# Performance work log

Hardware: AMD Instinct MI355X
Metric: run time of the kernel (lower is better)

Reference implementation:

```python
import jax, jax.numpy as jnp
import numpy as np

B, L, D, H, DK, DV = 2, 2048, 512, 8, 64, 64
EPS = 1e-6


def setup_inputs() -> dict:
    key = jax.random.key(0)
    ks = jax.random.split(key, 19)
    n = lambda k, s: jax.random.normal(k, s, dtype=jnp.float32)
    inp = {
        "q_r": n(ks[0], (B, L, D)), "q_i": n(ks[1], (B, L, D)),
        "k_r": n(ks[2], (B, L, D)), "k_i": n(ks[3], (B, L, D)),
        "v_r": n(ks[4], (B, L, D)), "v_i": n(ks[5], (B, L, D)),
        "wq_r": n(ks[6], (D, H * DK)) * 0.02, "wq_i": n(ks[7], (D, H * DK)) * 0.02,
        "wk_r": n(ks[8], (D, H * DK)) * 0.02, "wk_i": n(ks[9], (D, H * DK)) * 0.02,
        "wv_r": n(ks[10], (D, H * DV)) * 0.02, "wv_i": n(ks[11], (D, H * DV)) * 0.02,
        "wo_r": n(ks[12], (H * DV, D)) * 0.02, "wo_i": n(ks[13], (H * DV, D)) * 0.02,
        "ln_wr": n(ks[14], (D,)), "ln_wi": n(ks[15], (D,)),
        "ln_br": n(ks[16], (D,)), "ln_bi": n(ks[17], (D,)),
        "mask": jax.random.randint(ks[18], (B, L, L), 0, 2).astype(jnp.int32),
    }
    return inp


def _clinear(xr, xi, wr, wi):
    # complex matmul (xr + i xi) @ (wr + i wi)
    return xr @ wr - xi @ wi, xi @ wr + xr @ wi


def _complex_layernorm(r, i, wr, wi, br, bi, eps=EPS):
    axes = (1, 2)  # normalize over all non-batch dims of [B, L, D]
    r = r - r.mean(axis=axes, keepdims=True)
    i = i - i.mean(axis=axes, keepdims=True)
    Crr = (r * r).mean(axis=axes, keepdims=True) + eps
    Cii = (i * i).mean(axis=axes, keepdims=True) + eps
    Cri = (r * i).mean(axis=axes, keepdims=True)
    s = jnp.sqrt(Crr * Cii - Cri * Cri)
    t = jnp.sqrt(Crr + Cii + 2.0 * s)
    inv_st = 1.0 / (s * t)
    Rrr = (Cii + s) * inv_st
    Rii = (Crr + s) * inv_st
    Rri = -Cri * inv_st
    nr = Rrr * r + Rri * i
    ni = Rii * i + Rri * r
    # affine: complex multiply by (wr + i wi), then add complex bias
    out_r = nr * wr - ni * wi + br
    out_i = nr * wi + ni * wr + bi
    return out_r, out_i


def reference(q_r, q_i, k_r, k_i, v_r, v_i,
              wq_r, wq_i, wk_r, wk_i, wv_r, wv_i, wo_r, wo_i,
              ln_wr, ln_wi, ln_br, ln_bi, mask):
    res_r, res_i = q_r, q_i
    qr, qi = _clinear(q_r, q_i, wq_r, wq_i)
    kr, ki = _clinear(k_r, k_i, wk_r, wk_i)
    vr, vi = _clinear(v_r, v_i, wv_r, wv_i)
    # [B, L, H*Dk] -> [B, H, L, Dk]
    tohead = lambda x, d: x.reshape(B, L, H, d).transpose(0, 2, 1, 3)
    qr, qi = tohead(qr, DK), tohead(qi, DK)
    kr, ki = tohead(kr, DK), tohead(ki, DK)
    vr, vi = tohead(vr, DV), tohead(vi, DV)
    temp = jnp.float32(DK) ** 0.5
    qr, qi = qr / temp, qi / temp
    # complex scores (q @ conj(k)^T): re + i*im
    sr = jnp.einsum('bhqd,bhkd->bhqk', qr, kr) + jnp.einsum('bhqd,bhkd->bhqk', qi, ki)
    si = jnp.einsum('bhqd,bhkd->bhqk', qi, kr) - jnp.einsum('bhqd,bhkd->bhqk', qr, ki)
    a = jnp.sqrt(sr * sr + si * si)  # abs of complex scores
    a = jnp.where(mask[:, None, :, :] == 0, jnp.float32(-1e9), a)
    attn = jax.nn.softmax(a, axis=-1)  # real-valued attention weights
    out_r = jnp.einsum('bhqk,bhkd->bhqd', attn, vr)
    out_i = jnp.einsum('bhqk,bhkd->bhqd', attn, vi)
    # [B, H, L, Dv] -> [B, L, H*Dv]
    out_r = out_r.transpose(0, 2, 1, 3).reshape(B, L, H * DV)
    out_i = out_i.transpose(0, 2, 1, 3).reshape(B, L, H * DV)
    out_r, out_i = _clinear(out_r, out_i, wo_r, wo_i)
    out_r = out_r + res_r
    out_i = out_i + res_i
    out_r, out_i = _complex_layernorm(out_r, out_i, ln_wr, ln_wi, ln_br, ln_bi)
    return out_r, out_i, attn
```

## Files before the change

### kernel.cpp

```cpp
#include <hip/hip_runtime.h>

typedef unsigned short u16;
typedef unsigned int u32;
typedef unsigned long long u64;


typedef __attribute__((ext_vector_type(8))) short bf16x8;
typedef __attribute__((ext_vector_type(4))) float f32x4;
typedef __attribute__((ext_vector_type(4))) u32 u32x4;

__device__ __forceinline__ u16 f2bf(float f) {
  u32 x = __float_as_uint(f);
  return (u16)((x + 0x7FFFu + ((x >> 16) & 1u)) >> 16);
}
__device__ __forceinline__ u32 pk2(float a, float b) {
  return (u32)f2bf(a) | ((u32)f2bf(b) << 16);
}
__device__ __forceinline__ bf16x8 negv(bf16x8 v) {
  u32x4 x = __builtin_bit_cast(u32x4, v);
  x ^= 0x80008000u;
  return __builtin_bit_cast(bf16x8, x);
}

__global__ __launch_bounds__(256) void prep(
    const float* __restrict__ qr, const float* __restrict__ qi,
    const float* __restrict__ kr, const float* __restrict__ ki,
    const float* __restrict__ vr, const float* __restrict__ vi,
    const float* __restrict__ wqr, const float* __restrict__ wqi,
    const float* __restrict__ wkr, const float* __restrict__ wki,
    const float* __restrict__ wvr, const float* __restrict__ wvi,
    const float* __restrict__ wor, const float* __restrict__ woi,
    const int* __restrict__ mask,
    u16* __restrict__ A, u16* __restrict__ Btb, u64* __restrict__ mb,
    float* __restrict__ stats) {
  __shared__ float tile[64][65];
  int bid = blockIdx.x;
  int t = threadIdx.x;
  if (bid < 32768) {
    int tid = bid * 256 + t;
    u64 bal = __ballot(mask[tid] != 0);
    if ((t & 63) == 0) mb[tid >> 6] = bal;
    return;
  }
  bid -= 32768;
  if (bid < 6144) {
    int z = bid >> 11;
    int bx = bid & 2047;
    const float* r  = (z == 0) ? qr : (z == 1) ? kr : vr;
    const float* im = (z == 0) ? qi : (z == 1) ? ki : vi;
    int c = bx * 256 + t;
    int m = c >> 7;
    int ck = (c & 127) * 8;
    const float* s = (ck < 512) ? (r + (size_t)m * 512 + ck)
                                : (im + (size_t)m * 512 + (ck - 512));
    float4 a = ((const float4*)s)[0];
    float4 b = ((const float4*)s)[1];
    uint4 o;
    o.x = pk2(a.x, a.y); o.y = pk2(a.z, a.w);
    o.z = pk2(b.x, b.y); o.w = pk2(b.z, b.w);
    ((uint4*)(A + (size_t)z * 4194304))[c] = o;
    return;
  }
  bid -= 6144;
  if (bid < 1024) {
    int z = bid >> 8;
    int bx = bid & 255;
    const float* wr = (z==0)?wqr:(z==1)?wkr:(z==2)?wvr:wor;
    const float* wi = (z==0)?wqi:(z==1)?wki:(z==2)?wvi:woi;
    u16* Bt = Btb + (size_t)z * 1048576;
    int n0 = (bx >> 4) * 64;
    int k0 = (bx & 15) * 64;
    bool nlow = (n0 < 512), klow = (k0 < 512);
    const float* src = nlow ? (klow ? wr : wi) : (klow ? wi : wr);
    float sgn = (nlow && !klow) ? -1.0f : 1.0f;
    int col0 = nlow ? n0 : n0 - 512;
    int kr0 = klow ? k0 : k0 - 512;
    {
      int rr = t >> 2, cc = (t & 3) * 16;
      const float4* s = (const float4*)(src + (size_t)(kr0 + rr) * 512 + col0 + cc);
#pragma unroll
      for (int j = 0; j < 4; ++j) {
        float4 v = s[j];
        tile[rr][cc + j*4 + 0] = v.x; tile[rr][cc + j*4 + 1] = v.y;
        tile[rr][cc + j*4 + 2] = v.z; tile[rr][cc + j*4 + 3] = v.w;
      }
    }
    __syncthreads();
    {
      int nn = t >> 2, kc = (t & 3) * 16;
      u32 w[8];
#pragma unroll
      for (int j = 0; j < 8; ++j)
        w[j] = pk2(sgn * tile[kc + 2*j][nn], sgn * tile[kc + 2*j + 1][nn]);
      uint4* d = (uint4*)(Bt + (size_t)(n0 + nn) * 1024 + k0 + kc);
      d[0] = make_uint4(w[0], w[1], w[2], w[3]);
      d[1] = make_uint4(w[4], w[5], w[6], w[7]);
    }
    return;
  }
  if (t < 16) stats[t] = 0.0f;
}

__global__ __launch_bounds__(256) void pack_vt(const u16* __restrict__ Cvm,
                                               u16* __restrict__ vt) {
  int z = blockIdx.y;
  int b = z >> 3, h = z & 7;
  int lt = blockIdx.x >> 1, ct = blockIdx.x & 1;
  int l0 = lt * 64, c0 = ct * 64;
  int n0 = (ct == 0) ? (h * 64) : (512 + h * 64);
  __shared__ u16 tile[64][80];
  int t = threadIdx.x;
  {
    int lr = t >> 2, cc = (t & 3) * 16;
    const uint4* s = (const uint4*)(Cvm + ((size_t)(b * 2048 + l0 + lr)) * 1024 + n0 + cc);
    uint4 v0 = s[0], v1 = s[1];
    *(uint4*)&tile[lr][cc] = v0;
    *(uint4*)&tile[lr][cc + 8] = v1;
  }
  __syncthreads();
  {
    int cr = t >> 2, lc = (t & 3) * 16;
    u32 w[8];
#pragma unroll
    for (int j = 0; j < 8; ++j)
      w[j] = (u32)tile[lc + 2*j][cr] | ((u32)tile[lc + 2*j + 1][cr] << 16);
    uint4* d = (uint4*)(vt + ((size_t)z * 128 + c0 + cr) * 2048 + l0 + lc);
    d[0] = make_uint4(w[0], w[1], w[2], w[3]);
    d[1] = make_uint4(w[4], w[5], w[6], w[7]);
  }
}

__device__ __forceinline__ void glds128(const u16* __restrict__ g, int ld,
                                        u16* lds, int t) {
  int lane = t & 63, w = t >> 6;
  int sub = lane >> 3;
  int cs = (lane & 7) ^ sub;
#pragma unroll
  for (int p = 0; p < 4; ++p) {
    int r = p * 32 + w * 8 + sub;
    const u16* ga = g + (size_t)r * ld + cs * 8;
    u16* la = lds + (size_t)(p * 32 + w * 8) * 64;
    __builtin_amdgcn_global_load_lds(
        (const __attribute__((address_space(1))) void*)ga,
        (__attribute__((address_space(3))) void*)la, 16, 0, 0);
  }
}
__device__ __forceinline__ void glds64(const u16* __restrict__ g, int ld,
                                       u16* lds, int t) {
  int lane = t & 63, w = t >> 6;
  int sub = lane >> 3;
  int cs = (lane & 7) ^ sub;
#pragma unroll
  for (int p = 0; p < 2; ++p) {
    int r = p * 32 + w * 8 + sub;
    const u16* ga = g + (size_t)r * ld + cs * 8;
    u16* la = lds + (size_t)(p * 32 + w * 8) * 64;
    __builtin_amdgcn_global_load_lds(
        (const __attribute__((address_space(1))) void*)ga,
        (__attribute__((address_space(3))) void*)la, 16, 0, 0);
  }
}

__global__ __launch_bounds__(256) void gemm_proj(const u16* __restrict__ Abase,
                                                 const u16* __restrict__ Btbase,
                                                 u16* __restrict__ Cbase) {
  __shared__ u16 lA[128 * 64], lB[128 * 64];
  int t = threadIdx.x, lane = t & 63, wid = t >> 6;
  int c15 = lane & 15, g = lane >> 4, l7 = lane & 7;
  int z = blockIdx.z;
  const u16* A  = Abase  + (size_t)z * 4194304;
  const u16* Bt = Btbase + (size_t)z * 1048576;
  u16* C = Cbase + (size_t)z * 4194304;
  int brow = blockIdx.y * 128, bcol = blockIdx.x * 128;
  float scale = (z == 0) ? 0.125f : 1.0f;
  int sw0 = ((g ^ l7) << 3), sw1 = (((4 | g) ^ l7) << 3);
  int wr0 = (wid >> 1) * 64 + c15, wc0 = (wid & 1) * 64 + c15;
  const u16 *pA0 = lA + wr0 * 64 + sw0, *pA1 = lA + wr0 * 64 + sw1;
  const u16 *pB0 = lB + wc0 * 64 + sw0, *pB1 = lB + wc0 * 64 + sw1;
  f32x4 zero = {0.f, 0.f, 0.f, 0.f};
  f32x4 acc[4][4];
#pragma unroll
  for (int mi = 0; mi < 4; ++mi)
#pragma unroll
    for (int ni = 0; ni < 4; ++ni) acc[mi][ni] = zero;
  for (int kt = 0; kt < 1024; kt += 64) {
    glds128(A + (size_t)brow * 1024 + kt, 1024, lA, t);
    glds128(Bt + (size_t)bcol * 1024 + kt, 1024, lB, t);
    __syncthreads();
#pragma unroll
    for (int ks = 0; ks < 2; ++ks) {
      const u16* pa = ks ? pA1 : pA0;
      const u16* pb = ks ? pB1 : pB0;
      bf16x8 fa[4], fb[4];
#pragma unroll
      for (int i2 = 0; i2 < 4; ++i2) {
        fa[i2] = *(const bf16x8*)(pa + i2 * 1024);
        fb[i2] = *(const bf16x8*)(pb + i2 * 1024);
      }
#pragma unroll
      for (int mi = 0; mi < 4; ++mi)
#pragma unroll
        for (int ni = 0; ni < 4; ++ni)
          acc[mi][ni] = __builtin_amdgcn_mfma_f32_16x16x32_bf16(
              fa[mi], fb[ni], acc[mi][ni], 0, 0, 0);
    }
    __syncthreads();
  }
  int wrb = (wid >> 1) * 64, wcb = (wid & 1) * 64;
  int rj = g * 4, cj = c15;
#pragma unroll
  for (int mi = 0; mi < 4; ++mi)
#pragma unroll
    for (int ni = 0; ni < 4; ++ni)
#pragma unroll
      for (int j = 0; j < 4; ++j)
        C[(size_t)(brow + wrb + mi * 16 + rj + j) * 1024 +
          (bcol + wcb + ni * 16 + cj)] = f2bf(acc[mi][ni][j] * scale);
}

__global__ __launch_bounds__(256, 3) void fused_p1(
    const u16* __restrict__ Cq, const u16* __restrict__ Ck,
    const u16* __restrict__ vt, const u64* __restrict__ mb,
    float* __restrict__ invbuf, u16* __restrict__ Ao) {
  __shared__ u16 lKr[64 * 64], lKi[64 * 64], lV[128 * 64], lP[64 * 64];
  int t = threadIdx.x, lane = t & 63, w = t >> 6;
  int c15 = lane & 15, g = lane >> 4, l7 = lane & 7;
  int f = blockIdx.x + (int)gridDim.x * blockIdx.y;
  int wk = (f & 7) * 64 + (f >> 3);
  int strip = wk & 31, z = wk >> 5;
  int b = z >> 3, h = z & 7;
  int q0 = strip * 64;
  int arow = w * 16 + c15;
  int rbase = w * 16 + (g << 2);

  const u16* Qrow = Cq + ((size_t)(b * 2048 + q0 + arow)) * 1024 + h * 64;
  bf16x8 q0r = *(const bf16x8*)(Qrow + g * 8);
  bf16x8 q1r = *(const bf16x8*)(Qrow + 32 + g * 8);
  bf16x8 q0i = *(const bf16x8*)(Qrow + 512 + g * 8);
  bf16x8 q1i = *(const bf16x8*)(Qrow + 544 + g * 8);
  bf16x8 nq0r = negv(q0r), nq1r = negv(q1r);

  int sw0 = ((g ^ l7) << 3), sw1 = (((4 | g) ^ l7) << 3);
  const u16 *pKr0 = lKr + c15 * 64 + sw0, *pKr1 = lKr + c15 * 64 + sw1;
  const u16 *pKi0 = lKi + c15 * 64 + sw0, *pKi1 = lKi + c15 * 64 + sw1;
  const u16 *pV0 = lV + c15 * 64 + sw0, *pV1 = lV + c15 * 64 + sw1;
  const u16 *pP0 = lP + arow * 64 + sw0, *pP1 = lP + arow * 64 + sw1;

  size_t mbase = ((size_t)(b * 2048 + q0 + rbase)) * 32;
  float s[4] = {0.f, 0.f, 0.f, 0.f};
  f32x4 zero = {0.f, 0.f, 0.f, 0.f};
  f32x4 o[8];
#pragma unroll
  for (int ni = 0; ni < 8; ++ni) o[ni] = zero;

  const u16* Kb = Ck + ((size_t)(b * 2048)) * 1024 + h * 64;
  const u16* Vb = vt + (size_t)z * 262144;

  for (int tl = 0; tl < 32; ++tl) {
    int l0 = tl * 64;
    if (tl) __syncthreads();
    glds64(Kb + (size_t)l0 * 1024, 1024, lKr, t);
    glds64(Kb + (size_t)l0 * 1024 + 512, 1024, lKi, t);
    glds128(Vb + l0, 2048, lV, t);
    __syncthreads();
    f32x4 sr[4], si[4];
#pragma unroll
    for (int ni = 0; ni < 4; ++ni) { sr[ni] = zero; si[ni] = zero; }
#pragma unroll
    for (int ni = 0; ni < 4; ++ni) {
      bf16x8 g0 = *(const bf16x8*)(pKr0 + ni * 1024);
      bf16x8 g1 = *(const bf16x8*)(pKi0 + ni * 1024);
      sr[ni] = __builtin_amdgcn_mfma_f32_16x16x32_bf16(q0r, g0, sr[ni], 0, 0, 0);
      sr[ni] = __builtin_amdgcn_mfma_f32_16x16x32_bf16(q0i, g1, sr[ni], 0, 0, 0);
      si[ni] = __builtin_amdgcn_mfma_f32_16x16x32_bf16(q0i, g0, si[ni], 0, 0, 0);
      si[ni] = __builtin_amdgcn_mfma_f32_16x16x32_bf16(nq0r, g1, si[ni], 0, 0, 0);
      bf16x8 h0 = *(const bf16x8*)(pKr1 + ni * 1024);
      bf16x8 h1 = *(const bf16x8*)(pKi1 + ni * 1024);
      sr[ni] = __builtin_amdgcn_mfma_f32_16x16x32_bf16(q1r, h0, sr[ni], 0, 0, 0);
      sr[ni] = __builtin_amdgcn_mfma_f32_16x16x32_bf16(q1i, h1, sr[ni], 0, 0, 0);
      si[ni] = __builtin_amdgcn_mfma_f32_16x16x32_bf16(q1i, h0, si[ni], 0, 0, 0);
      si[ni] = __builtin_amdgcn_mfma_f32_16x16x32_bf16(nq1r, h1, si[ni], 0, 0, 0);
    }
    u64 wm[4];
#pragma unroll
    for (int j = 0; j < 4; ++j) wm[j] = mb[mbase + (size_t)j * 32 + tl];
#pragma unroll
    for (int ni = 0; ni < 4; ++ni) {
      int cbit = ni * 16 + c15;
      int pchi = ni * 2 + (c15 >> 3);
#pragma unroll
      for (int j = 0; j < 4; ++j) {
        float n = sr[ni][j] * sr[ni][j] + si[ni][j] * si[ni][j];
        float p = __expf(__builtin_amdgcn_sqrtf(n));
        p = ((wm[j] >> cbit) & 1ull) ? p : 0.0f;
        s[j] += p;
        lP[(rbase + j) * 64 + ((pchi ^ (((g & 1) << 2) + j)) << 3) + l7] = f2bf(p);
      }
    }
    {
      bf16x8 fa0 = *(const bf16x8*)pP0;
      bf16x8 fa1 = *(const bf16x8*)pP1;
#pragma unroll
      for (int ni = 0; ni < 8; ++ni) {
        bf16x8 fb0 = *(const bf16x8*)(pV0 + ni * 1024);
        bf16x8 fb1 = *(const bf16x8*)(pV1 + ni * 1024);
        o[ni] = __builtin_amdgcn_mfma_f32_16x16x32_bf16(fa0, fb0, o[ni], 0, 0, 0);
        o[ni] = __builtin_amdgcn_mfma_f32_16x16x32_bf16(fa1, fb1, o[ni], 0, 0, 0);
      }
    }
  }
  float inv[4];
#pragma unroll
  for (int j = 0; j < 4; ++j) {
    float sj = s[j];
#pragma unroll
    for (int off = 1; off < 16; off <<= 1) sj += __shfl_xor(sj, off);
    inv[j] = 1.0f / sj;
  }
  if (c15 == 0) {
#pragma unroll
    for (int j = 0; j < 4; ++j)
      invbuf[z * 2048 + q0 + rbase + j] = inv[j];
  }
#pragma unroll
  for (int ni = 0; ni < 8; ++ni) {
    int c = ni * 16 + c15;
    int nout = (c < 64) ? (h * 64 + c) : (512 + h * 64 + (c - 64));
#pragma unroll
    for (int j = 0; j < 4; ++j)
      Ao[((size_t)(b * 2048 + q0 + rbase + j)) * 1024 + nout] =
          f2bf(o[ni][j] * inv[j]);
  }
}

__global__ __launch_bounds__(256, 3) void attn_p2(
    const u16* __restrict__ Cq, const u16* __restrict__ Ck,
    const u64* __restrict__ mb, const float* __restrict__ invbuf,
    float* __restrict__ attn) {
  __shared__ u16 lKr[64 * 64], lKi[64 * 64];
  int t = threadIdx.x, lane = t & 63, w = t >> 6;
  int c15 = lane & 15, g = lane >> 4, l7 = lane & 7;
  int f = blockIdx.x + (int)gridDim.x * blockIdx.y;
  int wk = (f & 7) * 256 + (f >> 3);
  int z = wk >> 7;
  int rem = wk & 127;
  int strip = rem >> 2, kc = rem & 3;
  int b = z >> 3, h = z & 7;
  int q0 = strip * 64;
  int arow = w * 16 + c15;
  int rbase = w * 16 + (g << 2);

  const u16* Qrow = Cq + ((size_t)(b * 2048 + q0 + arow)) * 1024 + h * 64;
  bf16x8 q0r = *(const bf16x8*)(Qrow + g * 8);
  bf16x8 q1r = *(const bf16x8*)(Qrow + 32 + g * 8);
  bf16x8 q0i = *(const bf16x8*)(Qrow + 512 + g * 8);
  bf16x8 q1i = *(const bf16x8*)(Qrow + 544 + g * 8);
  bf16x8 nq0r = negv(q0r), nq1r = negv(q1r);

  int sw0 = ((g ^ l7) << 3), sw1 = (((4 | g) ^ l7) << 3);
  const u16 *pKr0 = lKr + c15 * 64 + sw0, *pKr1 = lKr + c15 * 64 + sw1;
  const u16 *pKi0 = lKi + c15 * 64 + sw0, *pKi1 = lKi + c15 * 64 + sw1;

  size_t mbase = ((size_t)(b * 2048 + q0 + rbase)) * 32;
  float inv[4];
#pragma unroll
  for (int j = 0; j < 4; ++j) inv[j] = invbuf[z * 2048 + q0 + rbase + j];
  f32x4 zero = {0.f, 0.f, 0.f, 0.f};
  const u16* Kb = Ck + ((size_t)(b * 2048)) * 1024 + h * 64;
  float* arow_out = attn + ((size_t)z * 2048 + q0 + rbase) * 2048 + c15;

  for (int tt2 = 0; tt2 < 8; ++tt2) {
    int tl = kc * 8 + tt2;
    int l0 = tl * 64;
    if (tt2) __syncthreads();
    glds64(Kb + (size_t)l0 * 1024, 1024, lKr, t);
    glds64(Kb + (size_t)l0 * 1024 + 512, 1024, lKi, t);
    __syncthreads();
    f32x4 sr[4], si[4];
#pragma unroll
    for (int ni = 0; ni < 4; ++ni) { sr[ni] = zero; si[ni] = zero; }
#pragma unroll
    for (int ni = 0; ni < 4; ++ni) {
      bf16x8 g0 = *(const bf16x8*)(pKr0 + ni * 1024);
      bf16x8 g1 = *(const bf16x8*)(pKi0 + ni * 1024);
      sr[ni] = __builtin_amdgcn_mfma_f32_16x16x32_bf16(q0r, g0, sr[ni], 0, 0, 0);
      sr[ni] = __builtin_amdgcn_mfma_f32_16x16x32_bf16(q0i, g1, sr[ni], 0, 0, 0);
      si[ni] = __builtin_amdgcn_mfma_f32_16x16x32_bf16(q0i, g0, si[ni], 0, 0, 0);
      si[ni] = __builtin_amdgcn_mfma_f32_16x16x32_bf16(nq0r, g1, si[ni], 0, 0, 0);
      bf16x8 h0 = *(const bf16x8*)(pKr1 + ni * 1024);
      bf16x8 h1 = *(const bf16x8*)(pKi1 + ni * 1024);
      sr[ni] = __builtin_amdgcn_mfma_f32_16x16x32_bf16(q1r, h0, sr[ni], 0, 0, 0);
      sr[ni] = __builtin_amdgcn_mfma_f32_16x16x32_bf16(q1i, h1, sr[ni], 0, 0, 0);
      si[ni] = __builtin_amdgcn_mfma_f32_16x16x32_bf16(q1i, h0, si[ni], 0, 0, 0);
      si[ni] = __builtin_amdgcn_mfma_f32_16x16x32_bf16(nq1r, h1, si[ni], 0, 0, 0);
    }
    u64 wm[4];
#pragma unroll
    for (int j = 0; j < 4; ++j) wm[j] = mb[mbase + (size_t)j * 32 + tl];
    float* outp = arow_out + l0;
#pragma unroll
    for (int ni = 0; ni < 4; ++ni) {
      int cbit = ni * 16 + c15;
#pragma unroll
      for (int j = 0; j < 4; ++j) {
        float n = sr[ni][j] * sr[ni][j] + si[ni][j] * si[ni][j];
        float p = __expf(__builtin_amdgcn_sqrtf(n)) * inv[j];
        p = ((wm[j] >> cbit) & 1ull) ? p : 0.0f;
        outp[(size_t)j * 2048 + ni * 16] = p;
      }
    }
  }
}

__global__ __launch_bounds__(256) void gemm_oproj(
    const u16* __restrict__ A, const u16* __restrict__ Bt,
    const float* __restrict__ resR, const float* __restrict__ resI,
    float* __restrict__ outR, float* __restrict__ outI) {
  __shared__ u16 lA[128 * 64], lB[128 * 64];
  int t = threadIdx.x, lane = t & 63, wid = t >> 6;
  int c15 = lane & 15, g = lane >> 4, l7 = lane & 7;
  int brow = blockIdx.y * 128, bcol = blockIdx.x * 128;
  int sw0 = ((g ^ l7) << 3), sw1 = (((4 | g) ^ l7) << 3);
  int wr0 = (wid >> 1) * 64 + c15, wc0 = (wid & 1) * 64 + c15;
  const u16 *pA0 = lA + wr0 * 64 + sw0, *pA1 = lA + wr0 * 64 + sw1;
  const u16 *pB0 = lB + wc0 * 64 + sw0, *pB1 = lB + wc0 * 64 + sw1;
  f32x4 zero = {0.f, 0.f, 0.f, 0.f};
  f32x4 acc[4][4];
#pragma unroll
  for (int mi = 0; mi < 4; ++mi)
#pragma unroll
    for (int ni = 0; ni < 4; ++ni) acc[mi][ni] = zero;
  for (int kt = 0; kt < 1024; kt += 64) {
    glds128(A + (size_t)brow * 1024 + kt, 1024, lA, t);
    glds128(Bt + (size_t)bcol * 1024 + kt, 1024, lB, t);
    __syncthreads();
#pragma unroll
    for (int ks = 0; ks < 2; ++ks) {
      const u16* pa = ks ? pA1 : pA0;
      const u16* pb = ks ? pB1 : pB0;
      bf16x8 fa[4], fb[4];
#pragma unroll
      for (int i2 = 0; i2 < 4; ++i2) {
        fa[i2] = *(const bf16x8*)(pa + i2 * 1024);
        fb[i2] = *(const bf16x8*)(pb + i2 * 1024);
      }
#pragma unroll
      for (int mi = 0; mi < 4; ++mi)
#pragma unroll
        for (int ni = 0; ni < 4; ++ni)
          acc[mi][ni] = __builtin_amdgcn_mfma_f32_16x16x32_bf16(
              fa[mi], fb[ni], acc[mi][ni], 0, 0, 0);
    }
    __syncthreads();
  }
  int wrb = (wid >> 1) * 64, wcb = (wid & 1) * 64;
  int rj = g * 4, cj = c15;
#pragma unroll
  for (int mi = 0; mi < 4; ++mi)
#pragma unroll
    for (int ni = 0; ni < 4; ++ni)
#pragma unroll
      for (int j = 0; j < 4; ++j) {
        int row = brow + wrb + mi * 16 + rj + j;
        int col = bcol + wcb + ni * 16 + cj;
        float v = acc[mi][ni][j];
        if (col < 512)
          outR[(size_t)row * 512 + col] = v + resR[(size_t)row * 512 + col];
        else {
          int c2 = col - 512;
          outI[(size_t)row * 512 + c2] = v + resI[(size_t)row * 512 + c2];
        }
      }
}

__global__ __launch_bounds__(256) void ln_reduce(const float* __restrict__ outR,
                                                 const float* __restrict__ outI,
                                                 float* __restrict__ stats) {
  int b = blockIdx.y;
  int t = threadIdx.x;
  size_t base = (size_t)b * 1048576 + (size_t)blockIdx.x * 2048;
  float s0 = 0.f, s1 = 0.f, s2 = 0.f, s3 = 0.f, s4 = 0.f;
#pragma unroll
  for (int p = 0; p < 8; ++p) {
    size_t e = base + p * 256 + t;
    float r = outR[e], i = outI[e];
    s0 += r; s1 += i; s2 += r * r; s3 += i * i; s4 += r * i;
  }
#pragma unroll
  for (int off = 32; off; off >>= 1) {
    s0 += __shfl_xor(s0, off); s1 += __shfl_xor(s1, off);
    s2 += __shfl_xor(s2, off); s3 += __shfl_xor(s3, off);
    s4 += __shfl_xor(s4, off);
  }
  __shared__ float red[4][5];
  if ((t & 63) == 0) {
    int w = t >> 6;
    red[w][0] = s0; red[w][1] = s1; red[w][2] = s2; red[w][3] = s3; red[w][4] = s4;
  }
  __syncthreads();
  if (t == 0) {
    float a0 = red[0][0] + red[1][0] + red[2][0] + red[3][0];
    float a1 = red[0][1] + red[1][1] + red[2][1] + red[3][1];
    float a2 = red[0][2] + red[1][2] + red[2][2] + red[3][2];
    float a3 = red[0][3] + red[1][3] + red[2][3] + red[3][3];
    float a4 = red[0][4] + red[1][4] + red[2][4] + red[3][4];
    atomicAdd(&stats[b * 8 + 0], a0);
    atomicAdd(&stats[b * 8 + 1], a1);
    atomicAdd(&stats[b * 8 + 2], a2);
    atomicAdd(&stats[b * 8 + 3], a3);
    atomicAdd(&stats[b * 8 + 4], a4);
  }
}

__global__ __launch_bounds__(256) void ln_apply(
    float* __restrict__ outR, float* __restrict__ outI,
    const float* __restrict__ stats,
    const float* __restrict__ lnwr, const float* __restrict__ lnwi,
    const float* __restrict__ lnbr, const float* __restrict__ lnbi) {
  int b = blockIdx.y;
  const float* st = stats + b * 8;
  float iN = 1.0f / 1048576.0f;
  float mr = st[0] * iN, mi = st[1] * iN;
  float Crr = st[2] * iN - mr * mr + 1e-6f;
  float Cii = st[3] * iN - mi * mi + 1e-6f;
  float Cri = st[4] * iN - mr * mi;
  float s = sqrtf(fmaxf(Crr * Cii - Cri * Cri, 0.f));
  float tt = sqrtf(Crr + Cii + 2.f * s);
  float inv = 1.0f / (s * tt);
  float Rrr = (Cii + s) * inv, Rii = (Crr + s) * inv, Rri = -Cri * inv;
  size_t e = ((size_t)blockIdx.x * 256 + threadIdx.x) * 4;
  size_t idx = (size_t)b * 1048576 + e;
  int d = (int)(e & 511);
  float4 r4 = *(float4*)(outR + idx);
  float4 i4 = *(float4*)(outI + idx);
  float4 wr = *(const float4*)(lnwr + d);
  float4 wi = *(const float4*)(lnwi + d);
  float4 br = *(const float4*)(lnbr + d);
  float4 bi = *(const float4*)(lnbi + d);
  float4 orr, oii;
#pragma unroll
  for (int j = 0; j < 4; ++j) {
    float r = ((&r4.x)[j]) - mr;
    float i = ((&i4.x)[j]) - mi;
    float nr = Rrr * r + Rri * i;
    float ni = Rii * i + Rri * r;
    (&orr.x)[j] = nr * (&wr.x)[j] - ni * (&wi.x)[j] + (&br.x)[j];
    (&oii.x)[j] = nr * (&wi.x)[j] + ni * (&wr.x)[j] + (&bi.x)[j];
  }
  *(float4*)(outR + idx) = orr;
  *(float4*)(outI + idx) = oii;
}

extern "C" void kernel_launch(void* const* d_in, const int* in_sizes, int n_in,
                              void* d_out, int out_size, void* d_ws, size_t ws_size,
                              hipStream_t stream) {
  const float* q_r = (const float*)d_in[0];
  const float* q_i = (const float*)d_in[1];
  const float* k_r = (const float*)d_in[2];
  const float* k_i = (const float*)d_in[3];
  const float* v_r = (const float*)d_in[4];
  const float* v_i = (const float*)d_in[5];
  const float* wq_r = (const float*)d_in[6];
  const float* wq_i = (const float*)d_in[7];
  const float* wk_r = (const float*)d_in[8];
  const float* wk_i = (const float*)d_in[9];
  const float* wv_r = (const float*)d_in[10];
  const float* wv_i = (const float*)d_in[11];
  const float* wo_r = (const float*)d_in[12];
  const float* wo_i = (const float*)d_in[13];
  const float* ln_wr = (const float*)d_in[14];
  const float* ln_wi = (const float*)d_in[15];
  const float* ln_br = (const float*)d_in[16];
  const float* ln_bi = (const float*)d_in[17];
  const int* mask = (const int*)d_in[18];

  float* outR = (float*)d_out;
  float* outI = outR + 2097152;
  float* attn = outR + 4194304;

  char* ws = (char*)d_ws;
  u16* Aq = (u16*)ws;
  u16* Bt = (u16*)(ws + 25165824);
  u16* Cq = (u16*)(ws + 33554432);
  u16* Ck = Cq + 4194304;
  u16* Cv = Cq + 8388608;
  u16* vt = Aq;
  u16* Ao = (u16*)(ws + 58720256);
  u64* mb = (u64*)(ws + 67108864);
  float* stats = (float*)(ws + 69206016);
  float* invbuf = (float*)(ws + 69207040);

  prep<<<dim3(32768 + 6144 + 1024 + 1), 256, 0, stream>>>(
      q_r, q_i, k_r, k_i, v_r, v_i, wq_r, wq_i, wk_r, wk_i, wv_r, wv_i,
      wo_r, wo_i, mask, Aq, Bt, mb, stats);
  gemm_proj<<<dim3(8, 32, 3), 256, 0, stream>>>(Aq, Bt, Cq);
  pack_vt<<<dim3(64, 16), 256, 0, stream>>>(Cv, vt);
  fused_p1<<<dim3(32, 16), 256, 0, stream>>>(Cq, Ck, vt, mb, invbuf, Ao);
  attn_p2<<<dim3(128, 16), 256, 0, stream>>>(Cq, Ck, mb, invbuf, attn);
  gemm_oproj<<<dim3(8, 32), 256, 0, stream>>>(Ao, Bt + 3145728, q_r, q_i, outR, outI);
  ln_reduce<<<dim3(512, 2), 256, 0, stream>>>(outR, outI, stats);
  ln_apply<<<dim3(1024, 2), 256, 0, stream>>>(outR, outI, stats, ln_wr, ln_wi,
                                              ln_br, ln_bi);
}
```

Before: 338.1 us.

## Double-buffer K/V shared-memory tiles in attention kernels to prefetch next tile

Both attention passes now keep two LDS buffers for the K (and V) tiles. Each iteration issues the load for tile t+1 before computing on tile t, which replaces the two barriers per iteration with one. The aim is to hide global-to-LDS load latency behind the MFMA and softmax work. In exchange, LDS use roughly doubles, and fused_p1's launch bound drops from 3 to 2 blocks per CU, which lowers occupancy.

After: 339.4 us. No clear change (+0.4%).

```diff
diff --git a/kernel.cpp b/kernel.cpp
--- a/kernel.cpp
+++ b/kernel.cpp
@@ -218,11 +218,11 @@
           (bcol + wcb + ni * 16 + cj)] = f2bf(acc[mi][ni][j] * scale);
 }
 
-__global__ __launch_bounds__(256, 3) void fused_p1(
+__global__ __launch_bounds__(256, 2) void fused_p1(
     const u16* __restrict__ Cq, const u16* __restrict__ Ck,
     const u16* __restrict__ vt, const u64* __restrict__ mb,
     float* __restrict__ invbuf, u16* __restrict__ Ao) {
-  __shared__ u16 lKr[64 * 64], lKi[64 * 64], lV[128 * 64], lP[64 * 64];
+  __shared__ u16 lKr[2][4096], lKi[2][4096], lV[2][8192], lP[4096];
   int t = threadIdx.x, lane = t & 63, w = t >> 6;
   int c15 = lane & 15, g = lane >> 4, l7 = lane & 7;
   int f = blockIdx.x + (int)gridDim.x * blockIdx.y;
@@ -241,9 +241,12 @@
   bf16x8 nq0r = negv(q0r), nq1r = negv(q1r);
 
   int sw0 = ((g ^ l7) << 3), sw1 = (((4 | g) ^ l7) << 3);
-  const u16 *pKr0 = lKr + c15 * 64 + sw0, *pKr1 = lKr + c15 * 64 + sw1;
-  const u16 *pKi0 = lKi + c15 * 64 + sw0, *pKi1 = lKi + c15 * 64 + sw1;
-  const u16 *pV0 = lV + c15 * 64 + sw0, *pV1 = lV + c15 * 64 + sw1;
+  const u16 *pKr0a = lKr[0] + c15 * 64 + sw0, *pKr1a = lKr[0] + c15 * 64 + sw1;
+  const u16 *pKr0b = lKr[1] + c15 * 64 + sw0, *pKr1b = lKr[1] + c15 * 64 + sw1;
+  const u16 *pKi0a = lKi[0] + c15 * 64 + sw0, *pKi1a = lKi[0] + c15 * 64 + sw1;
+  const u16 *pKi0b = lKi[1] + c15 * 64 + sw0, *pKi1b = lKi[1] + c15 * 64 + sw1;
+  const u16 *pV0a = lV[0] + c15 * 64 + sw0, *pV1a = lV[0] + c15 * 64 + sw1;
+  const u16 *pV0b = lV[1] + c15 * 64 + sw0, *pV1b = lV[1] + c15 * 64 + sw1;
   const u16 *pP0 = lP + arow * 64 + sw0, *pP1 = lP + arow * 64 + sw1;
 
   size_t mbase = ((size_t)(b * 2048 + q0 + rbase)) * 32;
@@ -256,26 +259,35 @@
   const u16* Kb = Ck + ((size_t)(b * 2048)) * 1024 + h * 64;
   const u16* Vb = vt + (size_t)z * 262144;
 
+  glds64(Kb, 1024, lKr[0], t);
+  glds64(Kb + 512, 1024, lKi[0], t);
+  glds128(Vb, 2048, lV[0], t);
+  __syncthreads();
+
   for (int tl = 0; tl < 32; ++tl) {
-    int l0 = tl * 64;
-    if (tl) __syncthreads();
-    glds64(Kb + (size_t)l0 * 1024, 1024, lKr, t);
-    glds64(Kb + (size_t)l0 * 1024 + 512, 1024, lKi, t);
-    glds128(Vb + l0, 2048, lV, t);
-    __syncthreads();
+    int cur = tl & 1;
+    if (tl < 31) {
+      size_t l1 = (size_t)(tl + 1) * 64;
+      glds64(Kb + l1 * 1024, 1024, lKr[cur ^ 1], t);
+      glds64(Kb + l1 * 1024 + 512, 1024, lKi[cur ^ 1], t);
+      glds128(Vb + l1, 2048, lV[cur ^ 1], t);
+    }
+    const u16 *kr0 = cur ? pKr0b : pKr0a, *kr1 = cur ? pKr1b : pKr1a;
+    const u16 *ki0 = cur ? pKi0b : pKi0a, *ki1 = cur ? pKi1b : pKi1a;
+    const u16 *v0p = cur ? pV0b : pV0a, *v1p = cur ? pV1b : pV1a;
     f32x4 sr[4], si[4];
 #pragma unroll
     for (int ni = 0; ni < 4; ++ni) { sr[ni] = zero; si[ni] = zero; }
 #pragma unroll
     for (int ni = 0; ni < 4; ++ni) {
-      bf16x8 g0 = *(const bf16x8*)(pKr0 + ni * 1024);
-      bf16x8 g1 = *(const bf16x8*)(pKi0 + ni * 1024);
+      bf16x8 g0 = *(const bf16x8*)(kr0 + ni * 1024);
+      bf16x8 g1 = *(const bf16x8*)(ki0 + ni * 1024);
       sr[ni] = __builtin_amdgcn_mfma_f32_16x16x32_bf16(q0r, g0, sr[ni], 0, 0, 0);
       sr[ni] = __builtin_amdgcn_mfma_f32_16x16x32_bf16(q0i, g1, sr[ni], 0, 0, 0);
       si[ni] = __builtin_amdgcn_mfma_f32_16x16x32_bf16(q0i, g0, si[ni], 0, 0, 0);
       si[ni] = __builtin_amdgcn_mfma_f32_16x16x32_bf16(nq0r, g1, si[ni], 0, 0, 0);
-      bf16x8 h0 = *(const bf16x8*)(pKr1 + ni * 1024);
-      bf16x8 h1 = *(const bf16x8*)(pKi1 + ni * 1024);
+      bf16x8 h0 = *(const bf16x8*)(kr1 + ni * 1024);
+      bf16x8 h1 = *(const bf16x8*)(ki1 + ni * 1024);
       sr[ni] = __builtin_amdgcn_mfma_f32_16x16x32_bf16(q1r, h0, sr[ni], 0, 0, 0);
       sr[ni] = __builtin_amdgcn_mfma_f32_16x16x32_bf16(q1i, h1, sr[ni], 0, 0, 0);
       si[ni] = __builtin_amdgcn_mfma_f32_16x16x32_bf16(q1i, h0, si[ni], 0, 0, 0);
@@ -302,12 +314,13 @@
       bf16x8 fa1 = *(const bf16x8*)pP1;
 #pragma unroll
       for (int ni = 0; ni < 8; ++ni) {
-        bf16x8 fb0 = *(const bf16x8*)(pV0 + ni * 1024);
-        bf16x8 fb1 = *(const bf16x8*)(pV1 + ni * 1024);
+        bf16x8 fb0 = *(const bf16x8*)(v0p + ni * 1024);
+        bf16x8 fb1 = *(const bf16x8*)(v1p + ni * 1024);
         o[ni] = __builtin_amdgcn_mfma_f32_16x16x32_bf16(fa0, fb0, o[ni], 0, 0, 0);
         o[ni] = __builtin_amdgcn_mfma_f32_16x16x32_bf16(fa1, fb1, o[ni], 0, 0, 0);
       }
     }
+    if (tl < 31) __syncthreads();
   }
   float inv[4];
 #pragma unroll
@@ -337,7 +350,7 @@
     const u16* __restrict__ Cq, const u16* __restrict__ Ck,
     const u64* __restrict__ mb, const float* __restrict__ invbuf,
     float* __restrict__ attn) {
-  __shared__ u16 lKr[64 * 64], lKi[64 * 64];
+  __shared__ u16 lKr[2][4096], lKi[2][4096];
   int t = threadIdx.x, lane = t & 63, w = t >> 6;
   int c15 = lane & 15, g = lane >> 4, l7 = lane & 7;
   int f = blockIdx.x + (int)gridDim.x * blockIdx.y;
@@ -358,8 +371,10 @@
   bf16x8 nq0r = negv(q0r), nq1r = negv(q1r);
 
   int sw0 = ((g ^ l7) << 3), sw1 = (((4 | g) ^ l7) << 3);
-  const u16 *pKr0 = lKr + c15 * 64 + sw0, *pKr1 = lKr + c15 * 64 + sw1;
-  const u16 *pKi0 = lKi + c15 * 64 + sw0, *pKi1 = lKi + c15 * 64 + sw1;
+  const u16 *pKr0a = lKr[0] + c15 * 64 + sw0, *pKr1a = lKr[0] + c15 * 64 + sw1;
+  const u16 *pKr0b = lKr[1] + c15 * 64 + sw0, *pKr1b = lKr[1] + c15 * 64 + sw1;
+  const u16 *pKi0a = lKi[0] + c15 * 64 + sw0, *pKi1a = lKi[0] + c15 * 64 + sw1;
+  const u16 *pKi0b = lKi[1] + c15 * 64 + sw0, *pKi1b = lKi[1] + c15 * 64 + sw1;
 
   size_t mbase = ((size_t)(b * 2048 + q0 + rbase)) * 32;
   float inv[4];
@@ -369,26 +384,37 @@
   const u16* Kb = Ck + ((size_t)(b * 2048)) * 1024 + h * 64;
   float* arow_out = attn + ((size_t)z * 2048 + q0 + rbase) * 2048 + c15;
 
+  {
+    size_t l0 = (size_t)(kc * 8) * 64;
+    glds64(Kb + l0 * 1024, 1024, lKr[0], t);
+    glds64(Kb + l0 * 1024 + 512, 1024, lKi[0], t);
+  }
+  __syncthreads();
+
   for (int tt2 = 0; tt2 < 8; ++tt2) {
     int tl = kc * 8 + tt2;
     int l0 = tl * 64;
-    if (tt2) __syncthreads();
-    glds64(Kb + (size_t)l0 * 1024, 1024, lKr, t);
-    glds64(Kb + (size_t)l0 * 1024 + 512, 1024, lKi, t);
-    __syncthreads();
+    int cur = tt2 & 1;
+    if (tt2 < 7) {
+      size_t l1 = (size_t)(tl + 1) * 64;
+      glds64(Kb + l1 * 1024, 1024, lKr[cur ^ 1], t);
+      glds64(Kb + l1 * 1024 + 512, 1024, lKi[cur ^ 1], t);
+    }
+    const u16 *kr0 = cur ? pKr0b : pKr0a, *kr1 = cur ? pKr1b : pKr1a;
+    const u16 *ki0 = cur ? pKi0b : pKi0a, *ki1 = cur ? pKi1b : pKi1a;
     f32x4 sr[4], si[4];
 #pragma unroll
     for (int ni = 0; ni < 4; ++ni) { sr[ni] = zero; si[ni] = zero; }
 #pragma unroll
     for (int ni = 0; ni < 4; ++ni) {
-      bf16x8 g0 = *(const bf16x8*)(pKr0 + ni * 1024);
-      bf16x8 g1 = *(const bf16x8*)(pKi0 + ni * 1024);
+      bf16x8 g0 = *(const bf16x8*)(kr0 + ni * 1024);
+      bf16x8 g1 = *(const bf16x8*)(ki0 + ni * 1024);
       sr[ni] = __builtin_amdgcn_mfma_f32_16x16x32_bf16(q0r, g0, sr[ni], 0, 0, 0);
       sr[ni] = __builtin_amdgcn_mfma_f32_16x16x32_bf16(q0i, g1, sr[ni], 0, 0, 0);
       si[ni] = __builtin_amdgcn_mfma_f32_16x16x32_bf16(q0i, g0, si[ni], 0, 0, 0);
       si[ni] = __builtin_amdgcn_mfma_f32_16x16x32_bf16(nq0r, g1, si[ni], 0, 0, 0);
-      bf16x8 h0 = *(const bf16x8*)(pKr1 + ni * 1024);
-      bf16x8 h1 = *(const bf16x8*)(pKi1 + ni * 1024);
+      bf16x8 h0 = *(const bf16x8*)(kr1 + ni * 1024);
+      bf16x8 h1 = *(const bf16x8*)(ki1 + ni * 1024);
       sr[ni] = __builtin_amdgcn_mfma_f32_16x16x32_bf16(q1r, h0, sr[ni], 0, 0, 0);
       sr[ni] = __builtin_amdgcn_mfma_f32_16x16x32_bf16(q1i, h1, sr[ni], 0, 0, 0);
       si[ni] = __builtin_amdgcn_mfma_f32_16x16x32_bf16(q1i, h0, si[ni], 0, 0, 0);
@@ -409,6 +435,7 @@
         outp[(size_t)j * 2048 + ni * 16] = p;
       }
     }
+    if (tt2 < 7) __syncthreads();
   }
 }
 
```

## Fuse V transpose into projection GEMM and co-schedule attn pass2 with output GEMM

Applied to the files above, without the earlier changes.

The V projection GEMM now writes its bf16 result straight into the transposed per-head vt layout, so the separate pack_vt kernel and its round trip through memory go away. The attention-probability pass and the output projection GEMM, which are independent of each other, are merged into one launch with a block-index split. The output GEMM blocks can then fill the GPU alongside the memory-bound attn writes, and one launch is saved. vt moves to a new workspace offset. The cost is scattered 8-byte transposed stores in the GEMM epilogue, and the merged kernel drops the occupancy hint of 3 blocks.

After: 355.8 us. 5.3% more time.

```diff
diff --git a/kernel.cpp b/kernel.cpp
--- a/kernel.cpp
+++ b/kernel.cpp
@@ -101,35 +101,6 @@
   if (t < 16) stats[t] = 0.0f;
 }
 
-__global__ __launch_bounds__(256) void pack_vt(const u16* __restrict__ Cvm,
-                                               u16* __restrict__ vt) {
-  int z = blockIdx.y;
-  int b = z >> 3, h = z & 7;
-  int lt = blockIdx.x >> 1, ct = blockIdx.x & 1;
-  int l0 = lt * 64, c0 = ct * 64;
-  int n0 = (ct == 0) ? (h * 64) : (512 + h * 64);
-  __shared__ u16 tile[64][80];
-  int t = threadIdx.x;
-  {
-    int lr = t >> 2, cc = (t & 3) * 16;
-    const uint4* s = (const uint4*)(Cvm + ((size_t)(b * 2048 + l0 + lr)) * 1024 + n0 + cc);
-    uint4 v0 = s[0], v1 = s[1];
-    *(uint4*)&tile[lr][cc] = v0;
-    *(uint4*)&tile[lr][cc + 8] = v1;
-  }
-  __syncthreads();
-  {
-    int cr = t >> 2, lc = (t & 3) * 16;
-    u32 w[8];
-#pragma unroll
-    for (int j = 0; j < 8; ++j)
-      w[j] = (u32)tile[lc + 2*j][cr] | ((u32)tile[lc + 2*j + 1][cr] << 16);
-    uint4* d = (uint4*)(vt + ((size_t)z * 128 + c0 + cr) * 2048 + l0 + lc);
-    d[0] = make_uint4(w[0], w[1], w[2], w[3]);
-    d[1] = make_uint4(w[4], w[5], w[6], w[7]);
-  }
-}
-
 __device__ __forceinline__ void glds128(const u16* __restrict__ g, int ld,
                                         u16* lds, int t) {
   int lane = t & 63, w = t >> 6;
@@ -163,7 +134,8 @@
 
 __global__ __launch_bounds__(256) void gemm_proj(const u16* __restrict__ Abase,
                                                  const u16* __restrict__ Btbase,
-                                                 u16* __restrict__ Cbase) {
+                                                 u16* __restrict__ Cbase,
+                                                 u16* __restrict__ vt) {
   __shared__ u16 lA[128 * 64], lB[128 * 64];
   int t = threadIdx.x, lane = t & 63, wid = t >> 6;
   int c15 = lane & 15, g = lane >> 4, l7 = lane & 7;
@@ -208,14 +180,32 @@
   }
   int wrb = (wid >> 1) * 64, wcb = (wid & 1) * 64;
   int rj = g * 4, cj = c15;
-#pragma unroll
-  for (int mi = 0; mi < 4; ++mi)
-#pragma unroll
-    for (int ni = 0; ni < 4; ++ni)
-#pragma unroll
-      for (int j = 0; j < 4; ++j)
-        C[(size_t)(brow + wrb + mi * 16 + rj + j) * 1024 +
-          (bcol + wcb + ni * 16 + cj)] = f2bf(acc[mi][ni][j] * scale);
+  if (z != 2) {
+#pragma unroll
+    for (int mi = 0; mi < 4; ++mi)
+#pragma unroll
+      for (int ni = 0; ni < 4; ++ni)
+#pragma unroll
+        for (int j = 0; j < 4; ++j)
+          C[(size_t)(brow + wrb + mi * 16 + rj + j) * 1024 +
+            (bcol + wcb + ni * 16 + cj)] = f2bf(acc[mi][ni][j] * scale);
+  } else {
+    int bq = brow >> 11;
+    int lq = (brow & 2047) + wrb + rj;
+#pragma unroll
+    for (int mi = 0; mi < 4; ++mi)
+#pragma unroll
+      for (int ni = 0; ni < 4; ++ni) {
+        int col = bcol + wcb + ni * 16 + cj;
+        int h = (col < 512) ? (col >> 6) : ((col - 512) >> 6);
+        int c = (col & 63) + ((col < 512) ? 0 : 64);
+        ushort4 v4;
+        v4.x = f2bf(acc[mi][ni][0]); v4.y = f2bf(acc[mi][ni][1]);
+        v4.z = f2bf(acc[mi][ni][2]); v4.w = f2bf(acc[mi][ni][3]);
+        *(ushort4*)(vt + ((size_t)((bq * 8 + h) * 128 + c)) * 2048 +
+                    lq + mi * 16) = v4;
+      }
+  }
 }
 
 __global__ __launch_bounds__(256, 3) void fused_p1(
@@ -333,144 +323,147 @@
   }
 }
 
-__global__ __launch_bounds__(256, 3) void attn_p2(
+__global__ __launch_bounds__(256) void tail_k(
     const u16* __restrict__ Cq, const u16* __restrict__ Ck,
     const u64* __restrict__ mb, const float* __restrict__ invbuf,
-    float* __restrict__ attn) {
-  __shared__ u16 lKr[64 * 64], lKi[64 * 64];
-  int t = threadIdx.x, lane = t & 63, w = t >> 6;
+    float* __restrict__ attn, const u16* __restrict__ Ao,
+    const u16* __restrict__ BtO, const float* __restrict__ resR,
+    const float* __restrict__ resI, float* __restrict__ outR,
+    float* __restrict__ outI) {
+  __shared__ u16 shm[16384];
+  int t = threadIdx.x, lane = t & 63;
   int c15 = lane & 15, g = lane >> 4, l7 = lane & 7;
-  int f = blockIdx.x + (int)gridDim.x * blockIdx.y;
-  int wk = (f & 7) * 256 + (f >> 3);
-  int z = wk >> 7;
-  int rem = wk & 127;
-  int strip = rem >> 2, kc = rem & 3;
-  int b = z >> 3, h = z & 7;
-  int q0 = strip * 64;
-  int arow = w * 16 + c15;
-  int rbase = w * 16 + (g << 2);
-
-  const u16* Qrow = Cq + ((size_t)(b * 2048 + q0 + arow)) * 1024 + h * 64;
-  bf16x8 q0r = *(const bf16x8*)(Qrow + g * 8);
-  bf16x8 q1r = *(const bf16x8*)(Qrow + 32 + g * 8);
-  bf16x8 q0i = *(const bf16x8*)(Qrow + 512 + g * 8);
-  bf16x8 q1i = *(const bf16x8*)(Qrow + 544 + g * 8);
-  bf16x8 nq0r = negv(q0r), nq1r = negv(q1r);
-
   int sw0 = ((g ^ l7) << 3), sw1 = (((4 | g) ^ l7) << 3);
-  const u16 *pKr0 = lKr + c15 * 64 + sw0, *pKr1 = lKr + c15 * 64 + sw1;
-  const u16 *pKi0 = lKi + c15 * 64 + sw0, *pKi1 = lKi + c15 * 64 + sw1;
-
-  size_t mbase = ((size_t)(b * 2048 + q0 + rbase)) * 32;
-  float inv[4];
-#pragma unroll
-  for (int j = 0; j < 4; ++j) inv[j] = invbuf[z * 2048 + q0 + rbase + j];
+  int f = blockIdx.x;
   f32x4 zero = {0.f, 0.f, 0.f, 0.f};
-  const u16* Kb = Ck + ((size_t)(b * 2048)) * 1024 + h * 64;
-  float* arow_out = attn + ((size_t)z * 2048 + q0 + rbase) * 2048 + c15;
-
-  for (int tt2 = 0; tt2 < 8; ++tt2) {
-    int tl = kc * 8 + tt2;
-    int l0 = tl * 64;
-    if (tt2) __syncthreads();
-    glds64(Kb + (size_t)l0 * 1024, 1024, lKr, t);
-    glds64(Kb + (size_t)l0 * 1024 + 512, 1024, lKi, t);
-    __syncthreads();
-    f32x4 sr[4], si[4];
-#pragma unroll
-    for (int ni = 0; ni < 4; ++ni) { sr[ni] = zero; si[ni] = zero; }
-#pragma unroll
-    for (int ni = 0; ni < 4; ++ni) {
-      bf16x8 g0 = *(const bf16x8*)(pKr0 + ni * 1024);
-      bf16x8 g1 = *(const bf16x8*)(pKi0 + ni * 1024);
-      sr[ni] = __builtin_amdgcn_mfma_f32_16x16x32_bf16(q0r, g0, sr[ni], 0, 0, 0);
-      sr[ni] = __builtin_amdgcn_mfma_f32_16x16x32_bf16(q0i, g1, sr[ni], 0, 0, 0);
-      si[ni] = __builtin_amdgcn_mfma_f32_16x16x32_bf16(q0i, g0, si[ni], 0, 0, 0);
-      si[ni] = __builtin_amdgcn_mfma_f32_16x16x32_bf16(nq0r, g1, si[ni], 0, 0, 0);
-      bf16x8 h0 = *(const bf16x8*)(pKr1 + ni * 1024);
-      bf16x8 h1 = *(const bf16x8*)(pKi1 + ni * 1024);
-      sr[ni] = __builtin_amdgcn_mfma_f32_16x16x32_bf16(q1r, h0, sr[ni], 0, 0, 0);
-      sr[ni] = __builtin_amdgcn_mfma_f32_16x16x32_bf16(q1i, h1, sr[ni], 0, 0, 0);
-      si[ni] = __builtin_amdgcn_mfma_f32_16x16x32_bf16(q1i, h0, si[ni], 0, 0, 0);
-      si[ni] = __builtin_amdgcn_mfma_f32_16x16x32_bf16(nq1r, h1, si[ni], 0, 0, 0);
-    }
-    u64 wm[4];
-#pragma unroll
-    for (int j = 0; j < 4; ++j) wm[j] = mb[mbase + (size_t)j * 32 + tl];
-    float* outp = arow_out + l0;
-#pragma unroll
-    for (int ni = 0; ni < 4; ++ni) {
-      int cbit = ni * 16 + c15;
-#pragma unroll
-      for (int j = 0; j < 4; ++j) {
-        float n = sr[ni][j] * sr[ni][j] + si[ni][j] * si[ni][j];
-        float p = __expf(__builtin_amdgcn_sqrtf(n)) * inv[j];
-        p = ((wm[j] >> cbit) & 1ull) ? p : 0.0f;
-        outp[(size_t)j * 2048 + ni * 16] = p;
-      }
-    }
-  }
-}
-
-__global__ __launch_bounds__(256) void gemm_oproj(
-    const u16* __restrict__ A, const u16* __restrict__ Bt,
-    const float* __restrict__ resR, const float* __restrict__ resI,
-    float* __restrict__ outR, float* __restrict__ outI) {
-  __shared__ u16 lA[128 * 64], lB[128 * 64];
-  int t = threadIdx.x, lane = t & 63, wid = t >> 6;
-  int c15 = lane & 15, g = lane >> 4, l7 = lane & 7;
-  int brow = blockIdx.y * 128, bcol = blockIdx.x * 128;
-  int sw0 = ((g ^ l7) << 3), sw1 = (((4 | g) ^ l7) << 3);
-  int wr0 = (wid >> 1) * 64 + c15, wc0 = (wid & 1) * 64 + c15;
-  const u16 *pA0 = lA + wr0 * 64 + sw0, *pA1 = lA + wr0 * 64 + sw1;
-  const u16 *pB0 = lB + wc0 * 64 + sw0, *pB1 = lB + wc0 * 64 + sw1;
-  f32x4 zero = {0.f, 0.f, 0.f, 0.f};
-  f32x4 acc[4][4];
-#pragma unroll
-  for (int mi = 0; mi < 4; ++mi)
-#pragma unroll
-    for (int ni = 0; ni < 4; ++ni) acc[mi][ni] = zero;
-  for (int kt = 0; kt < 1024; kt += 64) {
-    glds128(A + (size_t)brow * 1024 + kt, 1024, lA, t);
-    glds128(Bt + (size_t)bcol * 1024 + kt, 1024, lB, t);
-    __syncthreads();
-#pragma unroll
-    for (int ks = 0; ks < 2; ++ks) {
-      const u16* pa = ks ? pA1 : pA0;
-      const u16* pb = ks ? pB1 : pB0;
-      bf16x8 fa[4], fb[4];
-#pragma unroll
-      for (int i2 = 0; i2 < 4; ++i2) {
-        fa[i2] = *(const bf16x8*)(pa + i2 * 1024);
-        fb[i2] = *(const bf16x8*)(pb + i2 * 1024);
-      }
-#pragma unroll
-      for (int mi = 0; mi < 4; ++mi)
-#pragma unroll
-        for (int ni = 0; ni < 4; ++ni)
-          acc[mi][ni] = __builtin_amdgcn_mfma_f32_16x16x32_bf16(
-              fa[mi], fb[ni], acc[mi][ni], 0, 0, 0);
-    }
-    __syncthreads();
-  }
-  int wrb = (wid >> 1) * 64, wcb = (wid & 1) * 64;
-  int rj = g * 4, cj = c15;
-#pragma unroll
-  for (int mi = 0; mi < 4; ++mi)
-#pragma unroll
-    for (int ni = 0; ni < 4; ++ni)
-#pragma unroll
-      for (int j = 0; j < 4; ++j) {
-        int row = brow + wrb + mi * 16 + rj + j;
-        int col = bcol + wcb + ni * 16 + cj;
-        float v = acc[mi][ni][j];
-        if (col < 512)
-          outR[(size_t)row * 512 + col] = v + resR[(size_t)row * 512 + col];
-        else {
-          int c2 = col - 512;
-          outI[(size_t)row * 512 + c2] = v + resI[(size_t)row * 512 + c2];
+
+  if (f < 2048) {
+    int w = t >> 6;
+    u16* lKr = shm;
+    u16* lKi = shm + 4096;
+    int wk = (f & 7) * 256 + (f >> 3);
+    int z = wk >> 7;
+    int rem = wk & 127;
+    int strip = rem >> 2, kc = rem & 3;
+    int b = z >> 3, h = z & 7;
+    int q0 = strip * 64;
+    int arow = w * 16 + c15;
+    int rbase = w * 16 + (g << 2);
+
+    const u16* Qrow = Cq + ((size_t)(b * 2048 + q0 + arow)) * 1024 + h * 64;
+    bf16x8 q0r = *(const bf16x8*)(Qrow + g * 8);
+    bf16x8 q1r = *(const bf16x8*)(Qrow + 32 + g * 8);
+    bf16x8 q0i = *(const bf16x8*)(Qrow + 512 + g * 8);
+    bf16x8 q1i = *(const bf16x8*)(Qrow + 544 + g * 8);
+    bf16x8 nq0r = negv(q0r), nq1r = negv(q1r);
+
+    const u16 *pKr0 = lKr + c15 * 64 + sw0, *pKr1 = lKr + c15 * 64 + sw1;
+    const u16 *pKi0 = lKi + c15 * 64 + sw0, *pKi1 = lKi + c15 * 64 + sw1;
+
+    size_t mbase = ((size_t)(b * 2048 + q0 + rbase)) * 32;
+    float inv[4];
+#pragma unroll
+    for (int j = 0; j < 4; ++j) inv[j] = invbuf[z * 2048 + q0 + rbase + j];
+    const u16* Kb = Ck + ((size_t)(b * 2048)) * 1024 + h * 64;
+    float* arow_out = attn + ((size_t)z * 2048 + q0 + rbase) * 2048 + c15;
+
+    for (int tt2 = 0; tt2 < 8; ++tt2) {
+      int tl = kc * 8 + tt2;
+      int l0 = tl * 64;
+      if (tt2) __syncthreads();
+      glds64(Kb + (size_t)l0 * 1024, 1024, lKr, t);
+      glds64(Kb + (size_t)l0 * 1024 + 512, 1024, lKi, t);
+      __syncthreads();
+      f32x4 sr[4], si[4];
+#pragma unroll
+      for (int ni = 0; ni < 4; ++ni) { sr[ni] = zero; si[ni] = zero; }
+#pragma unroll
+      for (int ni = 0; ni < 4; ++ni) {
+        bf16x8 g0 = *(const bf16x8*)(pKr0 + ni * 1024);
+        bf16x8 g1 = *(const bf16x8*)(pKi0 + ni * 1024);
+        sr[ni] = __builtin_amdgcn_mfma_f32_16x16x32_bf16(q0r, g0, sr[ni], 0, 0, 0);
+        sr[ni] = __builtin_amdgcn_mfma_f32_16x16x32_bf16(q0i, g1, sr[ni], 0, 0, 0);
+        si[ni] = __builtin_amdgcn_mfma_f32_16x16x32_bf16(q0i, g0, si[ni], 0, 0, 0);
+        si[ni] = __builtin_amdgcn_mfma_f32_16x16x32_bf16(nq0r, g1, si[ni], 0, 0, 0);
+        bf16x8 h0 = *(const bf16x8*)(pKr1 + ni * 1024);
+        bf16x8 h1 = *(const bf16x8*)(pKi1 + ni * 1024);
+        sr[ni] = __builtin_amdgcn_mfma_f32_16x16x32_bf16(q1r, h0, sr[ni], 0, 0, 0);
+        sr[ni] = __builtin_amdgcn_mfma_f32_16x16x32_bf16(q1i, h1, sr[ni], 0, 0, 0);
+        si[ni] = __builtin_amdgcn_mfma_f32_16x16x32_bf16(q1i, h0, si[ni], 0, 0, 0);
+        si[ni] = __builtin_amdgcn_mfma_f32_16x16x32_bf16(nq1r, h1, si[ni], 0, 0, 0);
+      }
+      u64 wm[4];
+#pragma unroll
+      for (int j = 0; j < 4; ++j) wm[j] = mb[mbase + (size_t)j * 32 + tl];
+      float* outp = arow_out + l0;
+#pragma unroll
+      for (int ni = 0; ni < 4; ++ni) {
+        int cbit = ni * 16 + c15;
+#pragma unroll
+        for (int j = 0; j < 4; ++j) {
+          float n = sr[ni][j] * sr[ni][j] + si[ni][j] * si[ni][j];
+          float p = __expf(__builtin_amdgcn_sqrtf(n)) * inv[j];
+          p = ((wm[j] >> cbit) & 1ull) ? p : 0.0f;
+          outp[(size_t)j * 2048 + ni * 16] = p;
         }
       }
+    }
+  } else {
+    int bid2 = f - 2048;
+    int wid = t >> 6;
+    u16* lA = shm;
+    u16* lB = shm + 8192;
+    int brow = (bid2 >> 3) * 128, bcol = (bid2 & 7) * 128;
+    int wr0 = (wid >> 1) * 64 + c15, wc0 = (wid & 1) * 64 + c15;
+    const u16 *pA0 = lA + wr0 * 64 + sw0, *pA1 = lA + wr0 * 64 + sw1;
+    const u16 *pB0 = lB + wc0 * 64 + sw0, *pB1 = lB + wc0 * 64 + sw1;
+    f32x4 acc[4][4];
+#pragma unroll
+    for (int mi = 0; mi < 4; ++mi)
+#pragma unroll
+      for (int ni = 0; ni < 4; ++ni) acc[mi][ni] = zero;
+    for (int kt = 0; kt < 1024; kt += 64) {
+      glds128(Ao + (size_t)brow * 1024 + kt, 1024, lA, t);
+      glds128(BtO + (size_t)bcol * 1024 + kt, 1024, lB, t);
+      __syncthreads();
+#pragma unroll
+      for (int ks = 0; ks < 2; ++ks) {
+        const u16* pa = ks ? pA1 : pA0;
+        const u16* pb = ks ? pB1 : pB0;
+        bf16x8 fa[4], fb[4];
+#pragma unroll
+        for (int i2 = 0; i2 < 4; ++i2) {
+          fa[i2] = *(const bf16x8*)(pa + i2 * 1024);
+          fb[i2] = *(const bf16x8*)(pb + i2 * 1024);
+        }
+#pragma unroll
+        for (int mi = 0; mi < 4; ++mi)
+#pragma unroll
+          for (int ni = 0; ni < 4; ++ni)
+            acc[mi][ni] = __builtin_amdgcn_mfma_f32_16x16x32_bf16(
+                fa[mi], fb[ni], acc[mi][ni], 0, 0, 0);
+      }
+      __syncthreads();
+    }
+    int wrb = (wid >> 1) * 64, wcb = (wid & 1) * 64;
+    int rj = g * 4, cj = c15;
+#pragma unroll
+    for (int mi = 0; mi < 4; ++mi)
+#pragma unroll
+      for (int ni = 0; ni < 4; ++ni)
+#pragma unroll
+        for (int j = 0; j < 4; ++j) {
+          int row = brow + wrb + mi * 16 + rj + j;
+          int col = bcol + wcb + ni * 16 + cj;
+          float v = acc[mi][ni][j];
+          if (col < 512)
+            outR[(size_t)row * 512 + col] = v + resR[(size_t)row * 512 + col];
+          else {
+            int c2 = col - 512;
+            outI[(size_t)row * 512 + c2] = v + resI[(size_t)row * 512 + c2];
+          }
+        }
+  }
 }
 
 __global__ __launch_bounds__(256) void ln_reduce(const float* __restrict__ outR,
@@ -583,21 +576,19 @@
   u16* Bt = (u16*)(ws + 25165824);
   u16* Cq = (u16*)(ws + 33554432);
   u16* Ck = Cq + 4194304;
-  u16* Cv = Cq + 8388608;
-  u16* vt = Aq;
   u16* Ao = (u16*)(ws + 58720256);
   u64* mb = (u64*)(ws + 67108864);
   float* stats = (float*)(ws + 69206016);
   float* invbuf = (float*)(ws + 69207040);
+  u16* vt = (u16*)(ws + 75497472);
 
   prep<<<dim3(32768 + 6144 + 1024 + 1), 256, 0, stream>>>(
       q_r, q_i, k_r, k_i, v_r, v_i, wq_r, wq_i, wk_r, wk_i, wv_r, wv_i,
       wo_r, wo_i, mask, Aq, Bt, mb, stats);
-  gemm_proj<<<dim3(8, 32, 3), 256, 0, stream>>>(Aq, Bt, Cq);
-  pack_vt<<<dim3(64, 16), 256, 0, stream>>>(Cv, vt);
+  gemm_proj<<<dim3(8, 32, 3), 256, 0, stream>>>(Aq, Bt, Cq, vt);
   fused_p1<<<dim3(32, 16), 256, 0, stream>>>(Cq, Ck, vt, mb, invbuf, Ao);
-  attn_p2<<<dim3(128, 16), 256, 0, stream>>>(Cq, Ck, mb, invbuf, attn);
-  gemm_oproj<<<dim3(8, 32), 256, 0, stream>>>(Ao, Bt + 3145728, q_r, q_i, outR, outI);
+  tail_k<<<dim3(2304), 256, 0, stream>>>(Cq, Ck, mb, invbuf, attn, Ao,
+                                         Bt + 3145728, q_r, q_i, outR, outI);
   ln_reduce<<<dim3(512, 2), 256, 0, stream>>>(outR, outI, stats);
   ln_apply<<<dim3(1024, 2), 256, 0, stream>>>(outR, outI, stats, ln_wr, ln_wi,
                                               ln_br, ln_bi);
```
